# Kernel optimization log

Measured on AMD Instinct MI355X. Metric: run time of the kernel, lower is better.

## Reference

```python
import jax, jax.numpy as jnp
import numpy as np

B, I, H, O = 16384, 512, 1024, 512

def setup_inputs() -> dict:
    key = jax.random.key(0)
    ks = jax.random.split(key, 8)
    s_x = 1.0 / np.sqrt(I)
    s_h = 1.0 / np.sqrt(H)
    inp = jax.random.normal(ks[0], (B, I), jnp.float32)
    h = jax.random.normal(ks[1], (B, H), jnp.float32)
    c = jax.random.normal(ks[2], (B, H), jnp.float32)
    # stacked gate weights, order [i, o, f, z]
    Wx = jax.random.uniform(ks[3], (4, H, I), jnp.float32, -s_x, s_x)
    Wh = jax.random.uniform(ks[4], (4, H, H), jnp.float32, -s_h, s_h)
    # z-gate h2z weight is re-initialized with standard normal in reset_parameters
    Wh = Wh.at[3].set(jax.random.normal(ks[5], (H, H), jnp.float32))
    # biases per module init: i=linspace(-1,-10), o=0, f=linspace(1,10), z=0
    bx = jnp.stack([
        jnp.linspace(-1.0, -10.0, H, dtype=jnp.float32),
        jnp.zeros((H,), jnp.float32),
        jnp.linspace(1.0, 10.0, H, dtype=jnp.float32),
        jnp.zeros((H,), jnp.float32),
    ])
    Wout = jax.random.uniform(ks[6], (O, H), jnp.float32, -s_h, s_h)
    bout = jax.random.uniform(ks[7], (O,), jnp.float32, -s_h, s_h)
    return {"inp": inp, "h": h, "c": c, "Wx": Wx, "bx": bx, "Wh": Wh,
            "Wout": Wout, "bout": bout}

def reference(inp, h, c, Wx, bx, Wh, Wout, bout):
    # fused gate pre-activations: two stacked GEMMs
    # gx: [4, B, H], gh: [4, B, H]
    gx = jnp.einsum('bi,ghi->gbh', inp, Wx) + bx[:, None, :]
    gh = jnp.einsum('bh,gkh->gbk', h, Wh)
    g = gx + gh
    i = jax.nn.sigmoid(g[0])
    o = jax.nn.sigmoid(g[1])
    f = jax.nn.sigmoid(g[2])
    z = jnp.tanh(g[3])
    c_new = i * z + f * c
    h_new = o * jnp.tanh(c_new)  # act_fn = tanh
    out = h_new @ Wout.T + bout
    return (out, h_new)
```

## Files before the change

kernel.cpp:

```cpp
#include <hip/hip_runtime.h>
#include <stdint.h>

#define BB 16384
#define II 512
#define HH 1024
#define OO 512

typedef short s16x8 __attribute__((ext_vector_type(8)));
typedef float f32x4 __attribute__((ext_vector_type(4)));

__device__ __forceinline__ unsigned short f2bf(float x) {
  union { float f; unsigned u; } v; v.f = x;
  return (unsigned short)((v.u + 0x7fffu + ((v.u >> 16) & 1u)) >> 16);
}
__device__ __forceinline__ float bf2f(unsigned short b) {
  union { unsigned u; float f; } v; v.u = ((unsigned)b) << 16;
  return v.f;
}
__device__ __forceinline__ float sigmoid_f(float x) {
  return 1.0f / (1.0f + __expf(-x));
}
__device__ __forceinline__ float tanh_f(float x) {
  float ax = fabsf(x);
  float e = __expf(-2.0f * ax);
  float t = (1.0f - e) / (1.0f + e);
  return x >= 0.0f ? t : -t;
}

__device__ __forceinline__ void stage16(const void* g, void* l) {
  __builtin_amdgcn_global_load_lds((const __attribute__((address_space(1))) void*)g,
                                   (__attribute__((address_space(3))) void*)l,
                                   16, 0, 0);
}

__device__ __forceinline__ void mma_step64(const unsigned short* As, const unsigned short* Bs,
                                           f32x4 acc[4][4], int lane, int wave) {
  const int wm = wave & 1, wn = wave >> 1;
  const int ln = lane & 15, q = lane >> 4;
#pragma unroll
  for (int s = 0; s < 2; ++s) {
    s16x8 af[4], bfr[4];
#pragma unroll
    for (int i = 0; i < 4; ++i) {
      const int r = wm * 64 + i * 16 + ln;
      af[i] = *(const s16x8*)(As + r * 64 + ((((s << 2) + q) + r) & 7) * 8);
    }
#pragma unroll
    for (int i = 0; i < 4; ++i) {
      const int r = wn * 64 + i * 16 + ln;
      bfr[i] = *(const s16x8*)(Bs + r * 64 + ((((s << 2) + q) + r) & 7) * 8);
    }
#pragma unroll
    for (int mi = 0; mi < 4; ++mi)
#pragma unroll
      for (int ni = 0; ni < 4; ++ni)
        acc[mi][ni] = __builtin_amdgcn_mfma_f32_16x16x32_bf16(af[mi], bfr[ni], acc[mi][ni], 0, 0, 0);
  }
}


__global__ __launch_bounds__(256) void prep_X(const float* __restrict__ inp,
                                              const float* __restrict__ h,
                                              unsigned short* __restrict__ Xb,
                                              unsigned short* __restrict__ Hlo) {
  int t = blockIdx.x * 256 + threadIdx.x;
  int base = t * 8;
  int b = base / 1536;
  int k = base - b * 1536;
  const float* src = (k < 512) ? (inp + b * 512 + k) : (h + b * 1024 + (k - 512));
  float4 v0 = *(const float4*)src;
  float4 v1 = *(const float4*)(src + 4);
  float f[8] = {v0.x, v0.y, v0.z, v0.w, v1.x, v1.y, v1.z, v1.w};
  unsigned short hi[8];
#pragma unroll
  for (int i = 0; i < 8; ++i) hi[i] = f2bf(f[i]);
  *(s16x8*)(Xb + base) = *(s16x8*)hi;
  if (k >= 512) {
    unsigned short lo[8];
#pragma unroll
    for (int i = 0; i < 8; ++i) lo[i] = f2bf(f[i] - bf2f(hi[i]));
    *(s16x8*)(Hlo + b * 1024 + (k - 512)) = *(s16x8*)lo;
  }
}

__global__ __launch_bounds__(256) void prep_Wg(const float* __restrict__ Wx,
                                               const float* __restrict__ Wh,
                                               unsigned short* __restrict__ Wg) {
  int t = blockIdx.x * 256 + threadIdx.x;
  int base = t * 8;
  int n = base / 1536;
  int k = base - n * 1536;
  int r = n & 127;
  int gate = (r >> 4) & 3;
  int unit = ((n >> 7) << 5) + (((r >> 6) & 1) << 4) + (r & 15);
  const float* src = (k < 512) ? (Wx + (gate * 1024 + unit) * 512 + k)
                               : (Wh + (gate * 1024 + unit) * 1024 + (k - 512));
  float4 v0 = *(const float4*)src;
  float4 v1 = *(const float4*)(src + 4);
  float f[8] = {v0.x, v0.y, v0.z, v0.w, v1.x, v1.y, v1.z, v1.w};
  unsigned short o[8];
#pragma unroll
  for (int i = 0; i < 8; ++i) o[i] = f2bf(f[i]);
  *(s16x8*)(Wg + base) = *(s16x8*)o;
}

__global__ __launch_bounds__(256) void prep_Wz2(const float* __restrict__ Whz,
                                                unsigned short* __restrict__ Wz2) {
  int t = blockIdx.x * 256 + threadIdx.x;
  int base = t * 8;
  int n = base >> 11;
  int k = base & 2047;
  int klo = (k < 1024) ? k : (k - 1024);
  const float* src = Whz + n * 1024 + klo;
  float4 v0 = *(const float4*)src;
  float4 v1 = *(const float4*)(src + 4);
  float f[8] = {v0.x, v0.y, v0.z, v0.w, v1.x, v1.y, v1.z, v1.w};
  unsigned short o[8];
  if (k < 1024) {
#pragma unroll
    for (int i = 0; i < 8; ++i) { unsigned short h_ = f2bf(f[i]); o[i] = f2bf(f[i] - bf2f(h_)); }
  } else {
#pragma unroll
    for (int i = 0; i < 8; ++i) o[i] = f2bf(f[i]);
  }
  *(s16x8*)(Wz2 + base) = *(s16x8*)o;
}

__global__ __launch_bounds__(256) void prep_Wout(const float* __restrict__ Wout,
                                                 unsigned short* __restrict__ Wo) {
  int t = blockIdx.x * 256 + threadIdx.x;
  int base = t * 8;
  float4 v0 = *(const float4*)(Wout + base);
  float4 v1 = *(const float4*)(Wout + base + 4);
  float f[8] = {v0.x, v0.y, v0.z, v0.w, v1.x, v1.y, v1.z, v1.w};
  unsigned short o[8];
#pragma unroll
  for (int i = 0; i < 8; ++i) o[i] = f2bf(f[i]);
  *(s16x8*)(Wo + base) = *(s16x8*)o;
}


__global__ __launch_bounds__(256) void gemm_zcorr(const unsigned short* __restrict__ Xb,
                                                  const unsigned short* __restrict__ Hlo,
                                                  const unsigned short* __restrict__ Wz2,
                                                  unsigned short* __restrict__ Dgz) {
  __shared__ unsigned short As[8192];
  __shared__ unsigned short Bs[8192];
  const int n0 = blockIdx.x * 128;
  const int m0 = blockIdx.y * 128;
  const int tid = threadIdx.x, lane = tid & 63, wave = tid >> 6;
  const unsigned short *gaX[4], *gaH[4], *gb[4];
  unsigned short *la[4], *lb[4];
#pragma unroll
  for (int u = 0; u < 4; ++u) {
    int p = u * 256 + tid;
    int r = p >> 3;
    int j = ((p & 7) - r) & 7;
    gaX[u] = Xb + (size_t)(m0 + r) * 1536 + 512 + j * 8;
    gaH[u] = Hlo + (size_t)(m0 + r) * 1024 + j * 8;
    gb[u]  = Wz2 + (size_t)(n0 + r) * 2048 + j * 8;
    la[u] = As + (u * 256 + (tid & ~63)) * 8;
    lb[u] = Bs + (u * 256 + (tid & ~63)) * 8;
  }
  f32x4 acc[4][4] = {};
  for (int kk = 0; kk < 16; ++kk) {
#pragma unroll
    for (int u = 0; u < 4; ++u) { stage16(gaX[u], la[u]); stage16(gb[u], lb[u]); }
#pragma unroll
    for (int u = 0; u < 4; ++u) { gaX[u] += 64; gb[u] += 64; }
    __syncthreads();
    mma_step64(As, Bs, acc, lane, wave);
    __syncthreads();
  }
  for (int kk = 0; kk < 16; ++kk) {
#pragma unroll
    for (int u = 0; u < 4; ++u) { stage16(gaH[u], la[u]); stage16(gb[u], lb[u]); }
#pragma unroll
    for (int u = 0; u < 4; ++u) { gaH[u] += 64; gb[u] += 64; }
    __syncthreads();
    mma_step64(As, Bs, acc, lane, wave);
    __syncthreads();
  }
  const int wm = wave & 1, wn = wave >> 1;
  const int ln = lane & 15, q = lane >> 4;
#pragma unroll
  for (int mi = 0; mi < 4; ++mi) {
#pragma unroll
    for (int r = 0; r < 4; ++r) {
      const int b = m0 + wm * 64 + mi * 16 + q * 4 + r;
#pragma unroll
      for (int ni = 0; ni < 4; ++ni) {
        const int n = n0 + wn * 64 + ni * 16 + ln;
        Dgz[b * 1024 + n] = f2bf(acc[mi][ni][r]);
      }
    }
  }
}

__global__ __launch_bounds__(256) void gemm_gates(const unsigned short* __restrict__ Xb,
                                                   const unsigned short* __restrict__ Wg,
                                                   const float* __restrict__ bx,
                                                   const float* __restrict__ cold,
                                                   const unsigned short* __restrict__ Dgz,
                                                   float* __restrict__ hnew,
                                                   unsigned short* __restrict__ hnewb) {
  __shared__ unsigned short As[8192];
  __shared__ unsigned short Bs[8192];
  const int n0 = blockIdx.x * 128;
  const int m0 = blockIdx.y * 128;
  const int tid = threadIdx.x, lane = tid & 63, wave = tid >> 6;
  const unsigned short *ga[4], *gb[4];
  unsigned short *la[4], *lb[4];
#pragma unroll
  for (int u = 0; u < 4; ++u) {
    int p = u * 256 + tid;
    int r = p >> 3;
    int j = ((p & 7) - r) & 7;
    ga[u] = Xb + (size_t)(m0 + r) * 1536 + j * 8;
    gb[u] = Wg + (size_t)(n0 + r) * 1536 + j * 8;
    la[u] = As + (u * 256 + (tid & ~63)) * 8;
    lb[u] = Bs + (u * 256 + (tid & ~63)) * 8;
  }
  f32x4 acc[4][4] = {};
  for (int kk = 0; kk < 24; ++kk) {
#pragma unroll
    for (int u = 0; u < 4; ++u) { stage16(ga[u], la[u]); stage16(gb[u], lb[u]); }
#pragma unroll
    for (int u = 0; u < 4; ++u) { ga[u] += 64; gb[u] += 64; }
    __syncthreads();
    mma_step64(As, Bs, acc, lane, wave);
    __syncthreads();
  }
  const int wm = wave & 1, wn = wave >> 1;
  const int ln = lane & 15, q = lane >> 4;
  const int unit = (blockIdx.x << 5) + (wn << 4) + ln;
  const float bi = bx[unit];
  const float bo = bx[1024 + unit];
  const float bfg = bx[2048 + unit];
  const float bz = bx[3072 + unit];
#pragma unroll
  for (int mi = 0; mi < 4; ++mi) {
#pragma unroll
    for (int r = 0; r < 4; ++r) {
      const int b = m0 + wm * 64 + mi * 16 + q * 4 + r;
      const int idx = b * 1024 + unit;
      const float gi = acc[mi][0][r] + bi;
      const float go = acc[mi][1][r] + bo;
      const float gf = acc[mi][2][r] + bfg;
      const float gz = acc[mi][3][r] + bz + bf2f(Dgz[idx]);
      const float iv = sigmoid_f(gi);
      const float ov = sigmoid_f(go);
      const float fv = sigmoid_f(gf);
      const float zv = tanh_f(gz);
      const float cn = iv * zv + fv * cold[idx];
      const float hn = ov * tanh_f(cn);
      hnew[idx] = hn;
      hnewb[idx] = f2bf(hn);
    }
  }
}

__global__ __launch_bounds__(256) void gemm_out(const unsigned short* __restrict__ Hb,
                                                const unsigned short* __restrict__ Wo,
                                                const float* __restrict__ bout,
                                                float* __restrict__ out) {
  __shared__ unsigned short As[8192];
  __shared__ unsigned short Bs[8192];
  const int n0 = blockIdx.x * 128;
  const int m0 = blockIdx.y * 128;
  const int tid = threadIdx.x, lane = tid & 63, wave = tid >> 6;
  const unsigned short *ga[4], *gb[4];
  unsigned short *la[4], *lb[4];
#pragma unroll
  for (int u = 0; u < 4; ++u) {
    int p = u * 256 + tid;
    int r = p >> 3;
    int j = ((p & 7) - r) & 7;
    ga[u] = Hb + (size_t)(m0 + r) * 1024 + j * 8;
    gb[u] = Wo + (size_t)(n0 + r) * 1024 + j * 8;
    la[u] = As + (u * 256 + (tid & ~63)) * 8;
    lb[u] = Bs + (u * 256 + (tid & ~63)) * 8;
  }
  f32x4 acc[4][4] = {};
  for (int kk = 0; kk < 16; ++kk) {
#pragma unroll
    for (int u = 0; u < 4; ++u) { stage16(ga[u], la[u]); stage16(gb[u], lb[u]); }
#pragma unroll
    for (int u = 0; u < 4; ++u) { ga[u] += 64; gb[u] += 64; }
    __syncthreads();
    mma_step64(As, Bs, acc, lane, wave);
    __syncthreads();
  }
  const int wm = wave & 1, wn = wave >> 1;
  const int ln = lane & 15, q = lane >> 4;
  float bo_[4];
#pragma unroll
  for (int ni = 0; ni < 4; ++ni) bo_[ni] = bout[n0 + wn * 64 + ni * 16 + ln];
#pragma unroll
  for (int mi = 0; mi < 4; ++mi) {
#pragma unroll
    for (int r = 0; r < 4; ++r) {
      const int b = m0 + wm * 64 + mi * 16 + q * 4 + r;
#pragma unroll
      for (int ni = 0; ni < 4; ++ni) {
        const int n = n0 + wn * 64 + ni * 16 + ln;
        out[b * 512 + n] = acc[mi][ni][r] + bo_[ni];
      }
    }
  }
}

extern "C" void kernel_launch(void* const* d_in, const int* in_sizes, int n_in,
                              void* d_out, int out_size, void* d_ws, size_t ws_size,
                              hipStream_t stream) {
  const float* inp  = (const float*)d_in[0];
  const float* h    = (const float*)d_in[1];
  const float* c    = (const float*)d_in[2];
  const float* Wx   = (const float*)d_in[3];
  const float* bx   = (const float*)d_in[4];
  const float* Wh   = (const float*)d_in[5];
  const float* Wout = (const float*)d_in[6];
  const float* bout = (const float*)d_in[7];

  float* out  = (float*)d_out;
  float* hnew = out + (size_t)BB * OO;

  char* ws = (char*)d_ws;
  unsigned short* Xb  = (unsigned short*)(ws);
  unsigned short* Wg  = (unsigned short*)(ws + 50331648);
  unsigned short* Wo  = (unsigned short*)(ws + 62914560);
  unsigned short* Hb  = (unsigned short*)(ws + 63963136);
  unsigned short* Hlo = (unsigned short*)(ws + 97517568);
  unsigned short* Wz2 = (unsigned short*)(ws + 131072000);
  unsigned short* Dgz = (unsigned short*)(ws + 135266304);

  prep_X   <<<12288, 256, 0, stream>>>(inp, h, Xb, Hlo);
  prep_Wg  <<<3072,  256, 0, stream>>>(Wx, Wh, Wg);
  prep_Wz2 <<<1024,  256, 0, stream>>>(Wh + 3 * 1024 * 1024, Wz2);
  prep_Wout<<<256,   256, 0, stream>>>(Wout, Wo);
  gemm_zcorr<<<dim3(8, 128),  256, 0, stream>>>(Xb, Hlo, Wz2, Dgz);
  gemm_gates<<<dim3(32, 128), 256, 0, stream>>>(Xb, Wg, bx, c, Dgz, hnew, Hb);
  gemm_out  <<<dim3(4, 128),  256, 0, stream>>>(Hb, Wo, bout, out);
}
```

Before: 632.1 us.

## Rewrite gate and z-correction GEMMs as 256x256 double-buffered pipelined kernels

Replaces the 128x128 single-buffered gemm_gates and gemm_zcorr with 256x256-tile, 512-thread kernels. They double-buffer LDS, issue the next k-tile's global-to-LDS loads interleaved with MFMA phases using explicit vmcnt waits and barriers, and raise wave priority around MFMA bursts. The Wg prep layout changes to match the 64-unit-per-block gate interleave. This targets the exposed load latency and the low data reuse per tile, at the cost of 128KB of LDS per block and heavier register pressure from 8x4 accumulators.

```diff
diff --git a/kernel.cpp b/kernel.cpp
--- a/kernel.cpp
+++ b/kernel.cpp
@@ -90,9 +90,9 @@
   int base = t * 8;
   int n = base / 1536;
   int k = base - n * 1536;
-  int r = n & 127;
+  int r = n & 255;
   int gate = (r >> 4) & 3;
-  int unit = ((n >> 7) << 5) + (((r >> 6) & 1) << 4) + (r & 15);
+  int unit = ((n >> 8) << 6) + (((r >> 6) & 3) << 4) + (r & 15);
   const float* src = (k < 512) ? (Wx + (gate * 1024 + unit) * 512 + k)
                                : (Wh + (gate * 1024 + unit) * 1024 + (k - 512));
   float4 v0 = *(const float4*)src;
@@ -140,109 +140,136 @@
 }
 
 
-__global__ __launch_bounds__(256) void gemm_zcorr(const unsigned short* __restrict__ Xb,
-                                                  const unsigned short* __restrict__ Hlo,
-                                                  const unsigned short* __restrict__ Wz2,
-                                                  unsigned short* __restrict__ Dgz) {
-  __shared__ unsigned short As[8192];
-  __shared__ unsigned short Bs[8192];
-  const int n0 = blockIdx.x * 128;
-  const int m0 = blockIdx.y * 128;
-  const int tid = threadIdx.x, lane = tid & 63, wave = tid >> 6;
-  const unsigned short *gaX[4], *gaH[4], *gb[4];
-  unsigned short *la[4], *lb[4];
-#pragma unroll
-  for (int u = 0; u < 4; ++u) {
-    int p = u * 256 + tid;
-    int r = p >> 3;
-    int j = ((p & 7) - r) & 7;
-    gaX[u] = Xb + (size_t)(m0 + r) * 1536 + 512 + j * 8;
-    gaH[u] = Hlo + (size_t)(m0 + r) * 1024 + j * 8;
-    gb[u]  = Wz2 + (size_t)(n0 + r) * 2048 + j * 8;
-    la[u] = As + (u * 256 + (tid & ~63)) * 8;
-    lb[u] = Bs + (u * 256 + (tid & ~63)) * 8;
-  }
-  f32x4 acc[4][4] = {};
-  for (int kk = 0; kk < 16; ++kk) {
-#pragma unroll
-    for (int u = 0; u < 4; ++u) { stage16(gaX[u], la[u]); stage16(gb[u], lb[u]); }
-#pragma unroll
-    for (int u = 0; u < 4; ++u) { gaX[u] += 64; gb[u] += 64; }
-    __syncthreads();
-    mma_step64(As, Bs, acc, lane, wave);
-    __syncthreads();
-  }
-  for (int kk = 0; kk < 16; ++kk) {
-#pragma unroll
-    for (int u = 0; u < 4; ++u) { stage16(gaH[u], la[u]); stage16(gb[u], lb[u]); }
-#pragma unroll
-    for (int u = 0; u < 4; ++u) { gaH[u] += 64; gb[u] += 64; }
-    __syncthreads();
-    mma_step64(As, Bs, acc, lane, wave);
-    __syncthreads();
-  }
+#define RD_A(CA, MI, KS) (*(const s16x8*)((CA) + ((KS) ? aoff1 : aoff0) + (MI) * 1024))
+#define RD_B(CB, NI, KS) (*(const s16x8*)((CB) + ((KS) ? boff1 : boff0) + (NI) * 1024))
+#define VM4 asm volatile("s_waitcnt vmcnt(4)" ::: "memory")
+#define VM0 asm volatile("s_waitcnt vmcnt(0)" ::: "memory")
+#define VMNONE ((void)0)
+#define NOST ((void)0)
+
+#define ST_A(TT, HHX, DB) do { \
+  stage16(gA[HHX][0] + (TT) * 64, (DB) + (HHX) * 8192); \
+  stage16(gA[HHX][1] + (TT) * 64, (DB) + (HHX) * 8192 + 4096); } while (0)
+#define ST_B(TT, HHX, DB) do { \
+  stage16(gB[HHX][0] + (TT) * 64, (DB) + (HHX) * 8192); \
+  stage16(gB[HHX][1] + (TT) * 64, (DB) + (HHX) * 8192 + 4096); } while (0)
+#define ZST_A(TT, HHX, DB) do { \
+  const unsigned short* g0_; const unsigned short* g1_; \
+  if ((TT) < 16) { g0_ = gAX[HHX][0] + (TT) * 64; g1_ = gAX[HHX][1] + (TT) * 64; } \
+  else           { g0_ = gAH[HHX][0] + ((TT) - 16) * 64; g1_ = gAH[HHX][1] + ((TT) - 16) * 64; } \
+  stage16(g0_, (DB) + (HHX) * 8192); \
+  stage16(g1_, (DB) + (HHX) * 8192 + 4096); } while (0)
+
+#define PH_MFMA(Q, A00, A01, A10, A11) do { \
+  __builtin_amdgcn_s_barrier(); \
+  asm volatile("s_waitcnt lgkmcnt(0)" ::: "memory"); \
+  __builtin_amdgcn_s_setprio(1); \
+  _Pragma("unroll") \
+  for (int ni = 0; ni < 4; ++ni) { \
+    acc[2 * (Q)    ][ni] = __builtin_amdgcn_mfma_f32_16x16x32_bf16(A00, bq0[ni], acc[2 * (Q)    ][ni], 0, 0, 0); \
+    acc[2 * (Q) + 1][ni] = __builtin_amdgcn_mfma_f32_16x16x32_bf16(A01, bq0[ni], acc[2 * (Q) + 1][ni], 0, 0, 0); \
+  } \
+  _Pragma("unroll") \
+  for (int ni = 0; ni < 4; ++ni) { \
+    acc[2 * (Q)    ][ni] = __builtin_amdgcn_mfma_f32_16x16x32_bf16(A10, bq1[ni], acc[2 * (Q)    ][ni], 0, 0, 0); \
+    acc[2 * (Q) + 1][ni] = __builtin_amdgcn_mfma_f32_16x16x32_bf16(A11, bq1[ni], acc[2 * (Q) + 1][ni], 0, 0, 0); \
+  } \
+  __builtin_amdgcn_s_setprio(0); \
+} while (0)
+
+#define KTILE(CA, CB, S0, S1, S2, S3, VMX) do { \
+  s16x8 bq0[4], bq1[4]; \
+  _Pragma("unroll") \
+  for (int ni = 0; ni < 4; ++ni) { bq0[ni] = RD_B(CB, ni, 0); bq1[ni] = RD_B(CB, ni, 1); } \
+  s16x8 a00 = RD_A(CA, 0, 0), a01 = RD_A(CA, 1, 0); \
+  s16x8 a10 = RD_A(CA, 0, 1), a11 = RD_A(CA, 1, 1); \
+  S0; \
+  PH_MFMA(0, a00, a01, a10, a11); \
+  __builtin_amdgcn_s_barrier(); \
+  a00 = RD_A(CA, 2, 0); a01 = RD_A(CA, 3, 0); a10 = RD_A(CA, 2, 1); a11 = RD_A(CA, 3, 1); \
+  S1; \
+  PH_MFMA(1, a00, a01, a10, a11); \
+  __builtin_amdgcn_s_barrier(); \
+  a00 = RD_A(CA, 4, 0); a01 = RD_A(CA, 5, 0); a10 = RD_A(CA, 4, 1); a11 = RD_A(CA, 5, 1); \
+  S2; \
+  PH_MFMA(2, a00, a01, a10, a11); \
+  __builtin_amdgcn_s_barrier(); \
+  a00 = RD_A(CA, 6, 0); a01 = RD_A(CA, 7, 0); a10 = RD_A(CA, 6, 1); a11 = RD_A(CA, 7, 1); \
+  S3; \
+  PH_MFMA(3, a00, a01, a10, a11); \
+  VMX; \
+  __builtin_amdgcn_s_barrier(); \
+} while (0)
+
+__global__ __launch_bounds__(512, 2) void gemm_gates2(const unsigned short* __restrict__ Xb,
+                                                      const unsigned short* __restrict__ Wg,
+                                                      const float* __restrict__ bx,
+                                                      const float* __restrict__ cold,
+                                                      const unsigned short* __restrict__ Dgz,
+                                                      float* __restrict__ hnew,
+                                                      unsigned short* __restrict__ hnewb) {
+  __shared__ unsigned short lds[2][2][16384];
+  const int tid = threadIdx.x;
+  const int lane = tid & 63, wave = tid >> 6;
   const int wm = wave & 1, wn = wave >> 1;
-  const int ln = lane & 15, q = lane >> 4;
-#pragma unroll
-  for (int mi = 0; mi < 4; ++mi) {
-#pragma unroll
-    for (int r = 0; r < 4; ++r) {
-      const int b = m0 + wm * 64 + mi * 16 + q * 4 + r;
-#pragma unroll
-      for (int ni = 0; ni < 4; ++ni) {
-        const int n = n0 + wn * 64 + ni * 16 + ln;
-        Dgz[b * 1024 + n] = f2bf(acc[mi][ni][r]);
-      }
-    }
-  }
-}
-
-__global__ __launch_bounds__(256) void gemm_gates(const unsigned short* __restrict__ Xb,
-                                                   const unsigned short* __restrict__ Wg,
-                                                   const float* __restrict__ bx,
-                                                   const float* __restrict__ cold,
-                                                   const unsigned short* __restrict__ Dgz,
-                                                   float* __restrict__ hnew,
-                                                   unsigned short* __restrict__ hnewb) {
-  __shared__ unsigned short As[8192];
-  __shared__ unsigned short Bs[8192];
-  const int n0 = blockIdx.x * 128;
-  const int m0 = blockIdx.y * 128;
-  const int tid = threadIdx.x, lane = tid & 63, wave = tid >> 6;
-  const unsigned short *ga[4], *gb[4];
-  unsigned short *la[4], *lb[4];
-#pragma unroll
-  for (int u = 0; u < 4; ++u) {
-    int p = u * 256 + tid;
-    int r = p >> 3;
-    int j = ((p & 7) - r) & 7;
-    ga[u] = Xb + (size_t)(m0 + r) * 1536 + j * 8;
-    gb[u] = Wg + (size_t)(n0 + r) * 1536 + j * 8;
-    la[u] = As + (u * 256 + (tid & ~63)) * 8;
-    lb[u] = Bs + (u * 256 + (tid & ~63)) * 8;
-  }
-  f32x4 acc[4][4] = {};
-  for (int kk = 0; kk < 24; ++kk) {
-#pragma unroll
-    for (int u = 0; u < 4; ++u) { stage16(ga[u], la[u]); stage16(gb[u], lb[u]); }
-#pragma unroll
-    for (int u = 0; u < 4; ++u) { ga[u] += 64; gb[u] += 64; }
-    __syncthreads();
-    mma_step64(As, Bs, acc, lane, wave);
-    __syncthreads();
-  }
-  const int wm = wave & 1, wn = wave >> 1;
-  const int ln = lane & 15, q = lane >> 4;
-  const int unit = (blockIdx.x << 5) + (wn << 4) + ln;
+  const int ln = lane & 15, qlane = lane >> 4;
+  const int n0 = blockIdx.x << 8, m0 = blockIdx.y << 8;
+  const int sr = tid >> 3;
+  const int j = ((tid & 7) - (sr & 7)) & 7;
+
+  const unsigned short* gA[2][2];
+  const unsigned short* gB[2][2];
+#pragma unroll
+  for (int hh = 0; hh < 2; ++hh)
+#pragma unroll
+    for (int u = 0; u < 2; ++u) {
+      const int row = hh * 128 + u * 64 + sr;
+      gA[hh][u] = Xb + (size_t)(m0 + row) * 1536 + j * 8;
+      gB[hh][u] = Wg + (size_t)(n0 + row) * 1536 + j * 8;
+    }
+  unsigned short* const dA0 = &lds[0][0][0] + (tid & ~63) * 8;
+  unsigned short* const dB0 = &lds[0][1][0] + (tid & ~63) * 8;
+  unsigned short* const dA1 = &lds[1][0][0] + (tid & ~63) * 8;
+  unsigned short* const dB1 = &lds[1][1][0] + (tid & ~63) * 8;
+  const unsigned short* const lA0 = &lds[0][0][0];
+  const unsigned short* const lB0 = &lds[0][1][0];
+  const unsigned short* const lA1 = &lds[1][0][0];
+  const unsigned short* const lB1 = &lds[1][1][0];
+  const int sl0 = ((qlane + ln) & 7) * 8;
+  const int sl1 = sl0 ^ 32;
+  const int aoff0 = (wm * 128 + ln) * 64 + sl0;
+  const int aoff1 = (wm * 128 + ln) * 64 + sl1;
+  const int boff0 = (wn * 64 + ln) * 64 + sl0;
+  const int boff1 = (wn * 64 + ln) * 64 + sl1;
+
+  f32x4 acc[8][4] = {};
+
+  ST_A(0, 0, dA0); ST_A(0, 1, dA0);
+  ST_B(0, 0, dB0); ST_B(0, 1, dB0);
+  ST_B(1, 0, dB1); ST_B(1, 1, dB1);
+  VM4;
+  __builtin_amdgcn_s_barrier();
+
+#pragma unroll 1
+  for (int t = 0; t < 22; t += 2) {
+    KTILE(lA0, lB0, ST_A(t + 1, 0, dA1), ST_A(t + 1, 1, dA1),
+                    ST_B(t + 2, 0, dB0), ST_B(t + 2, 1, dB0), VM4);
+    KTILE(lA1, lB1, ST_A(t + 2, 0, dA0), ST_A(t + 2, 1, dA0),
+                    ST_B(t + 3, 0, dB1), ST_B(t + 3, 1, dB1), VM4);
+  }
+  KTILE(lA0, lB0, ST_A(23, 0, dA1), ST_A(23, 1, dA1), NOST, NOST, VM0);
+  KTILE(lA1, lB1, NOST, NOST, NOST, NOST, VMNONE);
+
+  const int unit = (blockIdx.x << 6) + (wn << 4) + ln;
   const float bi = bx[unit];
   const float bo = bx[1024 + unit];
   const float bfg = bx[2048 + unit];
   const float bz = bx[3072 + unit];
 #pragma unroll
-  for (int mi = 0; mi < 4; ++mi) {
+  for (int mi = 0; mi < 8; ++mi) {
 #pragma unroll
     for (int r = 0; r < 4; ++r) {
-      const int b = m0 + wm * 64 + mi * 16 + q * 4 + r;
+      const int b = m0 + wm * 128 + mi * 16 + qlane * 4 + r;
       const int idx = b * 1024 + unit;
       const float gi = acc[mi][0][r] + bi;
       const float go = acc[mi][1][r] + bo;
@@ -260,6 +287,78 @@
   }
 }
 
+__global__ __launch_bounds__(512, 2) void gemm_zcorr2(const unsigned short* __restrict__ Xb,
+                                                      const unsigned short* __restrict__ Hlo,
+                                                      const unsigned short* __restrict__ Wz2,
+                                                      unsigned short* __restrict__ Dgz) {
+  __shared__ unsigned short lds[2][2][16384];
+  const int tid = threadIdx.x;
+  const int lane = tid & 63, wave = tid >> 6;
+  const int wm = wave & 1, wn = wave >> 1;
+  const int ln = lane & 15, qlane = lane >> 4;
+  const int n0 = blockIdx.x << 8, m0 = blockIdx.y << 8;
+  const int sr = tid >> 3;
+  const int j = ((tid & 7) - (sr & 7)) & 7;
+
+  const unsigned short* gAX[2][2];
+  const unsigned short* gAH[2][2];
+  const unsigned short* gB[2][2];
+#pragma unroll
+  for (int hh = 0; hh < 2; ++hh)
+#pragma unroll
+    for (int u = 0; u < 2; ++u) {
+      const int row = hh * 128 + u * 64 + sr;
+      gAX[hh][u] = Xb  + (size_t)(m0 + row) * 1536 + 512 + j * 8;
+      gAH[hh][u] = Hlo + (size_t)(m0 + row) * 1024 + j * 8;
+      gB[hh][u]  = Wz2 + (size_t)(n0 + row) * 2048 + j * 8;
+    }
+  unsigned short* const dA0 = &lds[0][0][0] + (tid & ~63) * 8;
+  unsigned short* const dB0 = &lds[0][1][0] + (tid & ~63) * 8;
+  unsigned short* const dA1 = &lds[1][0][0] + (tid & ~63) * 8;
+  unsigned short* const dB1 = &lds[1][1][0] + (tid & ~63) * 8;
+  const unsigned short* const lA0 = &lds[0][0][0];
+  const unsigned short* const lB0 = &lds[0][1][0];
+  const unsigned short* const lA1 = &lds[1][0][0];
+  const unsigned short* const lB1 = &lds[1][1][0];
+  const int sl0 = ((qlane + ln) & 7) * 8;
+  const int sl1 = sl0 ^ 32;
+  const int aoff0 = (wm * 128 + ln) * 64 + sl0;
+  const int aoff1 = (wm * 128 + ln) * 64 + sl1;
+  const int boff0 = (wn * 64 + ln) * 64 + sl0;
+  const int boff1 = (wn * 64 + ln) * 64 + sl1;
+
+  f32x4 acc[8][4] = {};
+
+  ZST_A(0, 0, dA0); ZST_A(0, 1, dA0);
+  ST_B(0, 0, dB0);  ST_B(0, 1, dB0);
+  ST_B(1, 0, dB1);  ST_B(1, 1, dB1);
+  VM4;
+  __builtin_amdgcn_s_barrier();
+
+#pragma unroll 1
+  for (int t = 0; t < 30; t += 2) {
+    KTILE(lA0, lB0, ZST_A(t + 1, 0, dA1), ZST_A(t + 1, 1, dA1),
+                    ST_B(t + 2, 0, dB0),  ST_B(t + 2, 1, dB0), VM4);
+    KTILE(lA1, lB1, ZST_A(t + 2, 0, dA0), ZST_A(t + 2, 1, dA0),
+                    ST_B(t + 3, 0, dB1),  ST_B(t + 3, 1, dB1), VM4);
+  }
+  KTILE(lA0, lB0, ZST_A(31, 0, dA1), ZST_A(31, 1, dA1), NOST, NOST, VM0);
+  KTILE(lA1, lB1, NOST, NOST, NOST, NOST, VMNONE);
+
+#pragma unroll
+  for (int mi = 0; mi < 8; ++mi) {
+#pragma unroll
+    for (int r = 0; r < 4; ++r) {
+      const int b = m0 + wm * 128 + mi * 16 + qlane * 4 + r;
+#pragma unroll
+      for (int ni = 0; ni < 4; ++ni) {
+        const int n = n0 + wn * 64 + ni * 16 + ln;
+        Dgz[b * 1024 + n] = f2bf(acc[mi][ni][r]);
+      }
+    }
+  }
+}
+
 __global__ __launch_bounds__(256) void gemm_out(const unsigned short* __restrict__ Hb,
                                                 const unsigned short* __restrict__ Wo,
                                                 const float* __restrict__ bout,
@@ -275,9 +374,9 @@
   for (int u = 0; u < 4; ++u) {
     int p = u * 256 + tid;
     int r = p >> 3;
-    int j = ((p & 7) - r) & 7;
-    ga[u] = Hb + (size_t)(m0 + r) * 1024 + j * 8;
-    gb[u] = Wo + (size_t)(n0 + r) * 1024 + j * 8;
+    int jj = ((p & 7) - r) & 7;
+    ga[u] = Hb + (size_t)(m0 + r) * 1024 + jj * 8;
+    gb[u] = Wo + (size_t)(n0 + r) * 1024 + jj * 8;
     la[u] = As + (u * 256 + (tid & ~63)) * 8;
     lb[u] = Bs + (u * 256 + (tid & ~63)) * 8;
   }
@@ -338,7 +437,7 @@
   prep_Wg  <<<3072,  256, 0, stream>>>(Wx, Wh, Wg);
   prep_Wz2 <<<1024,  256, 0, stream>>>(Wh + 3 * 1024 * 1024, Wz2);
   prep_Wout<<<256,   256, 0, stream>>>(Wout, Wo);
-  gemm_zcorr<<<dim3(8, 128),  256, 0, stream>>>(Xb, Hlo, Wz2, Dgz);
-  gemm_gates<<<dim3(32, 128), 256, 0, stream>>>(Xb, Wg, bx, c, Dgz, hnew, Hb);
+  gemm_zcorr2<<<dim3(4, 64),  512, 0, stream>>>(Xb, Hlo, Wz2, Dgz);
+  gemm_gates2<<<dim3(16, 64), 512, 0, stream>>>(Xb, Wg, bx, c, Dgz, hnew, Hb);
   gemm_out  <<<dim3(4, 128),  256, 0, stream>>>(Hb, Wo, bout, out);
 }
```

Result: faster. 556.2 us (-12.0%).
